# Kernel tuning notes

Measured on AMD Instinct MI355X. Metric: run time of the kernel, lower is better.

## Reference

```python
import jax, jax.numpy as jnp
import numpy as np

DIM = 768
HEADS = 12
HEAD_DIM = DIM // HEADS
SCALE = HEAD_DIM ** -0.5


def setup_inputs() -> dict:
    key = jax.random.key(0)
    ks = jax.random.split(key, 9)
    B, N, M, C = 4, 1024, 1024, DIM
    std = C ** -0.5
    return {
        "q": jax.random.normal(ks[0], (B, N, C), jnp.float32),
        "k": jax.random.normal(ks[1], (B, M, C), jnp.float32),
        "v": jax.random.normal(ks[2], (B, M, C), jnp.float32),
        "mask": jax.random.uniform(ks[3], (B, N, M), jnp.float32),
        "Wq": jax.random.normal(ks[4], (C, C), jnp.float32) * std,
        "Wk": jax.random.normal(ks[5], (C, C), jnp.float32) * std,
        "Wv": jax.random.normal(ks[6], (C, C), jnp.float32) * std,
        "Wp": jax.random.normal(ks[7], (C, C), jnp.float32) * std,
        "bp": jax.random.normal(ks[8], (C,), jnp.float32) * 0.01,
    }


def reference(q, k, v, mask, Wq, Wk, Wv, Wp, bp):
    B, N, C = q.shape
    M = k.shape[1]
    H, D = HEADS, HEAD_DIM
    qh = (q @ Wq).reshape(B, N, H, D)
    kh = (k @ Wk).reshape(B, M, H, D)
    vh = (v @ Wv).reshape(B, M, H, D)
    attn = jnp.einsum('bnhd,bmhd->bhnm', qh, kh) * SCALE
    attn = jax.nn.softmax(attn, axis=-1)
    # post-softmax multiplicative mask, broadcast over heads
    attn = attn * mask[:, None, :, :]
    x = jnp.einsum('bhnm,bmhd->bnhd', attn, vh).reshape(B, N, C)
    return x @ Wp + bp
```

## Files before the change

### kernel.cpp

```cpp
#include <hip/hip_runtime.h>

typedef __bf16 bf16x8 __attribute__((ext_vector_type(8)));
typedef float f32x4 __attribute__((ext_vector_type(4)));

__device__ __forceinline__ unsigned short f2bf(float f) {
  union { float f; unsigned u; } x; x.f = f;
  unsigned r = x.u + 0x7FFFu + ((x.u >> 16) & 1u);
  return (unsigned short)(r >> 16);
}

__device__ __forceinline__ void gload_lds16(const void* g, void* l) {
  __builtin_amdgcn_global_load_lds(
      (const __attribute__((address_space(1))) unsigned int*)g,
      (__attribute__((address_space(3))) unsigned int*)l, 16, 0, 0);
}

__device__ __forceinline__ f32x4 mfma16(bf16x8 a, bf16x8 b, f32x4 c) {
  return __builtin_amdgcn_mfma_f32_16x16x32_bf16(a, b, c, 0, 0, 0);
}

__global__ __launch_bounds__(256) void conv_qkv(const float* __restrict__ q,
                                                const float* __restrict__ k,
                                                const float* __restrict__ v,
                                                unsigned short* __restrict__ dst) {
  const float* src = (blockIdx.y == 0) ? q : (blockIdx.y == 1 ? k : v);
  size_t i = ((size_t)blockIdx.x * 256 + threadIdx.x) * 4;
  float4 f = *(const float4*)(src + i);
  ushort4 u;
  u.x = f2bf(f.x); u.y = f2bf(f.y); u.z = f2bf(f.z); u.w = f2bf(f.w);
  *(ushort4*)(dst + (size_t)blockIdx.y * (4096u * 768u) + i) = u;
}

__global__ __launch_bounds__(256) void conv_w(const float* __restrict__ W0,
                                              const float* __restrict__ W1,
                                              const float* __restrict__ W2,
                                              const float* __restrict__ W3,
                                              unsigned short* __restrict__ Wt) {
  __shared__ float tile[32][33];
  const float* W = (blockIdx.z == 0) ? W0 : (blockIdx.z == 1) ? W1
                   : (blockIdx.z == 2) ? W2 : W3;
  int tx = threadIdx.x, ty = threadIdx.y;
  int n0 = blockIdx.x * 32, k0 = blockIdx.y * 32;
#pragma unroll
  for (int i = 0; i < 4; ++i)
    tile[ty * 4 + i][tx] = W[(size_t)(k0 + ty * 4 + i) * 768 + n0 + tx];
  __syncthreads();
  unsigned short* o = Wt + (size_t)blockIdx.z * 768 * 768;
#pragma unroll
  for (int i = 0; i < 4; ++i)
    o[(size_t)(n0 + ty * 4 + i) * 768 + k0 + tx] = f2bf(tile[tx][ty * 4 + i]);
}

__device__ __forceinline__ void gemm_core(const unsigned short* __restrict__ A,
                                          const unsigned short* __restrict__ B,
                                          unsigned short (*As)[64 * 64],
                                          unsigned short (*Bs)[128 * 64],
                                          int m0, int n0, int wm, int wn,
                                          int t, int g, int c16,
                                          f32x4 (&acc)[2][4]) {
  auto stageA = [&](unsigned short* dst, int k0) {
#pragma unroll
    for (int i = 0; i < 2; ++i) {
      int fc = i * 256 + t, r = fc >> 3, c = (fc & 7) ^ ((r >> 1) & 7);
      gload_lds16(A + (size_t)(m0 + r) * 768 + k0 + c * 8, (char*)dst + fc * 16);
    }
  };
  auto stageB = [&](unsigned short* dst, int k0) {
#pragma unroll
    for (int i = 0; i < 4; ++i) {
      int fc = i * 256 + t, r = fc >> 3, c = (fc & 7) ^ ((r >> 1) & 7);
      gload_lds16(B + (size_t)(n0 + r) * 768 + k0 + c * 8, (char*)dst + fc * 16);
    }
  };
  stageA(As[0], 0);
  stageB(Bs[0], 0);
  asm volatile("s_waitcnt vmcnt(0)" ::: "memory");
  __syncthreads();
  for (int s = 0; s < 12; ++s) {
    const int cur = s & 1;
    if (s < 11) {
      stageA(As[cur ^ 1], (s + 1) * 64);
      stageB(Bs[cur ^ 1], (s + 1) * 64);
    }
#pragma unroll
    for (int kk = 0; kk < 2; ++kk) {
      const int ch = kk * 4 + g;
      bf16x8 a[2], bw[4];
#pragma unroll
      for (int mi = 0; mi < 2; ++mi) {
        int r = wm + mi * 16 + c16;
        a[mi] = *(const bf16x8*)((char*)As[cur] + r * 128 + (((ch ^ (r >> 1)) & 7) << 4));
      }
#pragma unroll
      for (int ni = 0; ni < 4; ++ni) {
        int r = wn + ni * 16 + c16;
        bw[ni] = *(const bf16x8*)((char*)Bs[cur] + r * 128 + (((ch ^ (r >> 1)) & 7) << 4));
      }
#pragma unroll
      for (int mi = 0; mi < 2; ++mi)
#pragma unroll
        for (int ni = 0; ni < 4; ++ni)
          acc[mi][ni] = mfma16(a[mi], bw[ni], acc[mi][ni]);
    }
    __syncthreads();
  }
}

__global__ __launch_bounds__(256) void gemm_qkv(const unsigned short* __restrict__ Abase,
                                                const unsigned short* __restrict__ Wt,
                                                unsigned short* __restrict__ Hq,
                                                unsigned short* __restrict__ Hk,
                                                unsigned short* __restrict__ Hvt) {
  __shared__ unsigned short As[2][64 * 64], Bs[2][128 * 64];
  const int z = blockIdx.z;
  const unsigned short* A = Abase + (size_t)z * 4096 * 768;
  const unsigned short* B = Wt + (size_t)z * 768 * 768;
  const int t = threadIdx.x, l = t & 63, wid = t >> 6;
  const int g = l >> 4, c16 = l & 15;
  const int m0 = blockIdx.y * 64, n0 = blockIdx.x * 128;
  const int wm = (wid >> 1) * 32, wn = (wid & 1) * 64;
  f32x4 acc[2][4] = {};
  gemm_core(A, B, As, Bs, m0, n0, wm, wn, t, g, c16, acc);
  if (z < 2) {
    unsigned short* C = (z == 0) ? Hq : Hk;
#pragma unroll
    for (int mi = 0; mi < 2; ++mi)
#pragma unroll
      for (int ni = 0; ni < 4; ++ni) {
        int col = n0 + wn + ni * 16 + c16;
        int row = m0 + wm + mi * 16 + g * 4;
#pragma unroll
        for (int j = 0; j < 4; ++j)
          C[(size_t)(row + j) * 768 + col] = f2bf(acc[mi][ni][j]);
      }
  } else {
#pragma unroll
    for (int mi = 0; mi < 2; ++mi) {
      int rowbase = m0 + wm + mi * 16;
      int bat = rowbase >> 10;
      int mloc = (rowbase & 1023) + g * 4;
#pragma unroll
      for (int ni = 0; ni < 4; ++ni) {
        int col = n0 + wn + ni * 16 + c16;
        ushort4 u;
        u.x = f2bf(acc[mi][ni][0]); u.y = f2bf(acc[mi][ni][1]);
        u.z = f2bf(acc[mi][ni][2]); u.w = f2bf(acc[mi][ni][3]);
        *(ushort4*)(Hvt + (((size_t)(bat * 768 + col)) << 10) + mloc) = u;
      }
    }
  }
}

__global__ __launch_bounds__(256) void attn(const unsigned short* __restrict__ qh,
                                            const unsigned short* __restrict__ kh,
                                            const unsigned short* __restrict__ vhT,
                                            const float* __restrict__ mask,
                                            unsigned short* __restrict__ xb) {
  __shared__ unsigned short Ks[2][64 * 64], Vts[2][64 * 64], Ps[4 * 16 * 64];
  const int qt = blockIdx.x, h = blockIdx.y, b = blockIdx.z;
  const int t = threadIdx.x, l = t & 63, wid = t >> 6;
  const int g = l >> 4, c16 = l & 15;

  const unsigned short* qp =
      qh + ((size_t)(b * 1024 + qt * 64 + wid * 16 + c16)) * 768 + h * 64 + g * 8;
  bf16x8 aq0 = *(const bf16x8*)qp;
  bf16x8 aq1 = *(const bf16x8*)(qp + 32);

  const int fc0 = t, r0 = fc0 >> 3, c0 = (fc0 & 7) ^ ((r0 >> 1) & 7);
  const int fc1 = 256 + t, r1 = fc1 >> 3, c1 = (fc1 & 7) ^ ((r1 >> 1) & 7);
  const unsigned short* kp0 = kh + (size_t)(b * 1024 + r0) * 768 + h * 64 + c0 * 8;
  const unsigned short* kp1 = kh + (size_t)(b * 1024 + r1) * 768 + h * 64 + c1 * 8;
  const unsigned short* vp0 = vhT + ((size_t)(b * 768 + h * 64 + r0)) * 1024 + c0 * 8;
  const unsigned short* vp1 = vhT + ((size_t)(b * 768 + h * 64 + r1)) * 1024 + c1 * 8;
  gload_lds16(kp0, (char*)Ks[0] + fc0 * 16);
  gload_lds16(kp1, (char*)Ks[0] + fc1 * 16);
  gload_lds16(vp0, (char*)Vts[0] + fc0 * 16);
  gload_lds16(vp1, (char*)Vts[0] + fc1 * 16);
  kp0 += 64 * 768; kp1 += 64 * 768; vp0 += 64; vp1 += 64;

  const float* mrow0 =
      mask + ((size_t)(b * 1024 + qt * 64 + wid * 16 + g * 4)) * 1024 + c16;
  const float* mrow1 = mrow0 + 1024;
  const float* mrow2 = mrow0 + 2048;
  const float* mrow3 = mrow0 + 3072;

  asm volatile("s_waitcnt vmcnt(0)" ::: "memory");
  __syncthreads();

  f32x4 o[4] = {};
  float ls[4] = {0.f, 0.f, 0.f, 0.f};
  const float sc = 0.125f * 1.44269504088896341f;
  char* Pw = (char*)Ps + wid * 2048;

  for (int kv = 0; kv < 16; ++kv) {
    const int cur = kv & 1;
    if (kv < 15) {
      char* kd = (char*)Ks[cur ^ 1];
      char* vd = (char*)Vts[cur ^ 1];
      gload_lds16(kp0, kd + fc0 * 16);
      gload_lds16(kp1, kd + fc1 * 16);
      gload_lds16(vp0, vd + fc0 * 16);
      gload_lds16(vp1, vd + fc1 * 16);
      kp0 += 64 * 768; kp1 += 64 * 768; vp0 += 64; vp1 += 64;
    }
    float mreg[4][4];
#pragma unroll
    for (int ni = 0; ni < 4; ++ni) {
      mreg[ni][0] = mrow0[ni * 16];
      mreg[ni][1] = mrow1[ni * 16];
      mreg[ni][2] = mrow2[ni * 16];
      mreg[ni][3] = mrow3[ni * 16];
    }
    mrow0 += 64; mrow1 += 64; mrow2 += 64; mrow3 += 64;
    f32x4 p[4] = {};
#pragma unroll
    for (int kk = 0; kk < 2; ++kk) {
      const int ch = kk * 4 + g;
      bf16x8 aq = kk ? aq1 : aq0;
#pragma unroll
      for (int ni = 0; ni < 4; ++ni) {
        int r = ni * 16 + c16;
        bf16x8 bk = *(const bf16x8*)((char*)Ks[cur] + r * 128 + (((ch ^ (r >> 1)) & 7) << 4));
        p[ni] = mfma16(aq, bk, p[ni]);
      }
    }
#pragma unroll
    for (int j = 0; j < 4; ++j) {
      float e0 = exp2f(p[0][j] * sc);
      float e1 = exp2f(p[1][j] * sc);
      float e2 = exp2f(p[2][j] * sc);
      float e3 = exp2f(p[3][j] * sc);
      p[0][j] = e0; p[1][j] = e1; p[2][j] = e2; p[3][j] = e3;
      ls[j] += (e0 + e1) + (e2 + e3);
    }
#pragma unroll
    for (int ni = 0; ni < 4; ++ni)
#pragma unroll
      for (int j = 0; j < 4; ++j) {
        float pv = p[ni][j] * mreg[ni][j];
        int row = g * 4 + j, col = ni * 16 + c16;
        *(unsigned short*)(Pw + row * 128 +
                           ((((col >> 3) ^ (row >> 1)) & 7) << 4) + ((col & 7) << 1)) = f2bf(pv);
      }
    asm volatile("s_waitcnt lgkmcnt(0)" ::: "memory");
#pragma unroll
    for (int kk = 0; kk < 2; ++kk) {
      const int ch = kk * 4 + g;
      bf16x8 ap = *(const bf16x8*)(Pw + c16 * 128 + (((ch ^ (c16 >> 1)) & 7) << 4));
#pragma unroll
      for (int ni = 0; ni < 4; ++ni) {
        int r = ni * 16 + c16;
        bf16x8 bv = *(const bf16x8*)((char*)Vts[cur] + r * 128 + (((ch ^ (r >> 1)) & 7) << 4));
        o[ni] = mfma16(ap, bv, o[ni]);
      }
    }
    __syncthreads();
  }
#pragma unroll
  for (int j = 0; j < 4; ++j) {
    float s = ls[j];
    s += __shfl_xor(s, 1);
    s += __shfl_xor(s, 2);
    s += __shfl_xor(s, 4);
    s += __shfl_xor(s, 8);
    ls[j] = 1.0f / s;
  }
#pragma unroll
  for (int ni = 0; ni < 4; ++ni) {
    int col = h * 64 + ni * 16 + c16;
    int row = qt * 64 + wid * 16 + g * 4;
#pragma unroll
    for (int j = 0; j < 4; ++j)
      xb[((size_t)(b * 1024) + row + j) * 768 + col] = f2bf(o[ni][j] * ls[j]);
  }
}

__global__ __launch_bounds__(256) void gemm_proj(const unsigned short* __restrict__ A,
                                                 const unsigned short* __restrict__ B,
                                                 const float* __restrict__ bias,
                                                 float* __restrict__ C) {
  __shared__ unsigned short As[2][64 * 64], Bs[2][128 * 64];
  const int t = threadIdx.x, l = t & 63, wid = t >> 6;
  const int g = l >> 4, c16 = l & 15;
  const int m0 = blockIdx.y * 64, n0 = blockIdx.x * 128;
  const int wm = (wid >> 1) * 32, wn = (wid & 1) * 64;
  f32x4 acc[2][4] = {};
  gemm_core(A, B, As, Bs, m0, n0, wm, wn, t, g, c16, acc);
#pragma unroll
  for (int mi = 0; mi < 2; ++mi)
#pragma unroll
    for (int ni = 0; ni < 4; ++ni) {
      int col = n0 + wn + ni * 16 + c16;
      int row = m0 + wm + mi * 16 + g * 4;
      float bv = bias[col];
#pragma unroll
      for (int j = 0; j < 4; ++j)
        C[(size_t)(row + j) * 768 + col] = acc[mi][ni][j] + bv;
    }
}

extern "C" void kernel_launch(void* const* d_in, const int* in_sizes, int n_in,
                              void* d_out, int out_size, void* d_ws, size_t ws_size,
                              hipStream_t stream) {
  const float* q    = (const float*)d_in[0];
  const float* k    = (const float*)d_in[1];
  const float* v    = (const float*)d_in[2];
  const float* mask = (const float*)d_in[3];
  const float* Wq   = (const float*)d_in[4];
  const float* Wk   = (const float*)d_in[5];
  const float* Wv   = (const float*)d_in[6];
  const float* Wp   = (const float*)d_in[7];
  const float* bp   = (const float*)d_in[8];
  float* out = (float*)d_out;

  const size_t MN = (size_t)4096 * 768;
  const size_t WW = (size_t)768 * 768;
  unsigned short* qkv_bf = (unsigned short*)d_ws;
  unsigned short* wt     = qkv_bf + 3 * MN;
  unsigned short* heads  = wt + 4 * WW;
  unsigned short* xb     = heads + 3 * MN;

  conv_qkv<<<dim3(3072, 3), 256, 0, stream>>>(q, k, v, qkv_bf);
  conv_w<<<dim3(24, 24, 4), dim3(32, 8), 0, stream>>>(Wq, Wk, Wv, Wp, wt);
  gemm_qkv<<<dim3(6, 64, 3), 256, 0, stream>>>(qkv_bf, wt, heads, heads + MN, heads + 2 * MN);
  attn<<<dim3(16, 12, 4), 256, 0, stream>>>(heads, heads + MN, heads + 2 * MN, mask, xb);
  gemm_proj<<<dim3(6, 64), 256, 0, stream>>>(xb, wt + 3 * WW, bp, out);
}
```

Before: 102.8 us.

## Keep softmax probabilities in registers by transposing QK^T MFMA and permuting K rows

Swaps the MFMA operand order so S^T comes out in a register layout that can be packed straight into the A operand of the PV MFMA. K rows are loaded in a permuted order so the keys line up with that layout. This removes the per-iteration LDS write/read round trip through the P buffer. The softmax scale is folded into Q in the projection epilogue, and the mask is now read with vectorised float4 loads. The row-sum reduction is reworked with cross-lane shuffles to match the new layout, which adds index-permutation complexity and a risk of subtle layout errors.

```diff
diff --git a/kernel.cpp b/kernel.cpp
--- a/kernel.cpp
+++ b/kernel.cpp
@@ -17,6 +17,13 @@
 
 __device__ __forceinline__ f32x4 mfma16(bf16x8 a, bf16x8 b, f32x4 c) {
   return __builtin_amdgcn_mfma_f32_16x16x32_bf16(a, b, c, 0, 0, 0);
+}
+
+__device__ __forceinline__ bf16x8 pack8(const f32x4& a, const f32x4& b) {
+  bf16x8 r;
+  r[0] = (__bf16)a[0]; r[1] = (__bf16)a[1]; r[2] = (__bf16)a[2]; r[3] = (__bf16)a[3];
+  r[4] = (__bf16)b[0]; r[5] = (__bf16)b[1]; r[6] = (__bf16)b[2]; r[7] = (__bf16)b[3];
+  return r;
 }
 
 __global__ __launch_bounds__(256) void conv_qkv(const float* __restrict__ q,
@@ -122,6 +129,7 @@
   f32x4 acc[2][4] = {};
   gemm_core(A, B, As, Bs, m0, n0, wm, wn, t, g, c16, acc);
   if (z < 2) {
+    const float f = (z == 0) ? 0.125f * 1.44269504088896341f : 1.0f;
     unsigned short* C = (z == 0) ? Hq : Hk;
 #pragma unroll
     for (int mi = 0; mi < 2; ++mi)
@@ -131,7 +139,7 @@
         int row = m0 + wm + mi * 16 + g * 4;
 #pragma unroll
         for (int j = 0; j < 4; ++j)
-          C[(size_t)(row + j) * 768 + col] = f2bf(acc[mi][ni][j]);
+          C[(size_t)(row + j) * 768 + col] = f2bf(acc[mi][ni][j] * f);
       }
   } else {
 #pragma unroll
@@ -156,7 +164,7 @@
                                             const unsigned short* __restrict__ vhT,
                                             const float* __restrict__ mask,
                                             unsigned short* __restrict__ xb) {
-  __shared__ unsigned short Ks[2][64 * 64], Vts[2][64 * 64], Ps[4 * 16 * 64];
+  __shared__ unsigned short Ks[2][64 * 64], Vts[2][64 * 64];
   const int qt = blockIdx.x, h = blockIdx.y, b = blockIdx.z;
   const int t = threadIdx.x, l = t & 63, wid = t >> 6;
   const int g = l >> 4, c16 = l & 15;
@@ -168,8 +176,10 @@
 
   const int fc0 = t, r0 = fc0 >> 3, c0 = (fc0 & 7) ^ ((r0 >> 1) & 7);
   const int fc1 = 256 + t, r1 = fc1 >> 3, c1 = (fc1 & 7) ^ ((r1 >> 1) & 7);
-  const unsigned short* kp0 = kh + (size_t)(b * 1024 + r0) * 768 + h * 64 + c0 * 8;
-  const unsigned short* kp1 = kh + (size_t)(b * 1024 + r1) * 768 + h * 64 + c1 * 8;
+  const int s0 = 32 * (r0 >> 5) + 8 * ((r0 >> 2) & 3) + 4 * ((r0 >> 4) & 1) + (r0 & 3);
+  const int s1 = 32 * (r1 >> 5) + 8 * ((r1 >> 2) & 3) + 4 * ((r1 >> 4) & 1) + (r1 & 3);
+  const unsigned short* kp0 = kh + (size_t)(b * 1024 + s0) * 768 + h * 64 + c0 * 8;
+  const unsigned short* kp1 = kh + (size_t)(b * 1024 + s1) * 768 + h * 64 + c1 * 8;
   const unsigned short* vp0 = vhT + ((size_t)(b * 768 + h * 64 + r0)) * 1024 + c0 * 8;
   const unsigned short* vp1 = vhT + ((size_t)(b * 768 + h * 64 + r1)) * 1024 + c1 * 8;
   gload_lds16(kp0, (char*)Ks[0] + fc0 * 16);
@@ -178,19 +188,13 @@
   gload_lds16(vp1, (char*)Vts[0] + fc1 * 16);
   kp0 += 64 * 768; kp1 += 64 * 768; vp0 += 64; vp1 += 64;
 
-  const float* mrow0 =
-      mask + ((size_t)(b * 1024 + qt * 64 + wid * 16 + g * 4)) * 1024 + c16;
-  const float* mrow1 = mrow0 + 1024;
-  const float* mrow2 = mrow0 + 2048;
-  const float* mrow3 = mrow0 + 3072;
+  const float* mq = mask + ((size_t)(b * 1024 + qt * 64 + wid * 16 + c16)) * 1024 + 8 * g;
 
   asm volatile("s_waitcnt vmcnt(0)" ::: "memory");
   __syncthreads();
 
   f32x4 o[4] = {};
-  float ls[4] = {0.f, 0.f, 0.f, 0.f};
-  const float sc = 0.125f * 1.44269504088896341f;
-  char* Pw = (char*)Ps + wid * 2048;
+  f32x4 ls = {0.f, 0.f, 0.f, 0.f};
 
   for (int kv = 0; kv < 16; ++kv) {
     const int cur = kv & 1;
@@ -203,15 +207,12 @@
       gload_lds16(vp1, vd + fc1 * 16);
       kp0 += 64 * 768; kp1 += 64 * 768; vp0 += 64; vp1 += 64;
     }
-    float mreg[4][4];
-#pragma unroll
-    for (int ni = 0; ni < 4; ++ni) {
-      mreg[ni][0] = mrow0[ni * 16];
-      mreg[ni][1] = mrow1[ni * 16];
-      mreg[ni][2] = mrow2[ni * 16];
-      mreg[ni][3] = mrow3[ni * 16];
-    }
-    mrow0 += 64; mrow1 += 64; mrow2 += 64; mrow3 += 64;
+    const float* mk = mq + kv * 64;
+    f32x4 mreg[4];
+    mreg[0] = *(const f32x4*)(mk);
+    mreg[1] = *(const f32x4*)(mk + 4);
+    mreg[2] = *(const f32x4*)(mk + 32);
+    mreg[3] = *(const f32x4*)(mk + 36);
     f32x4 p[4] = {};
 #pragma unroll
     for (int kk = 0; kk < 2; ++kk) {
@@ -221,32 +222,27 @@
       for (int ni = 0; ni < 4; ++ni) {
         int r = ni * 16 + c16;
         bf16x8 bk = *(const bf16x8*)((char*)Ks[cur] + r * 128 + (((ch ^ (r >> 1)) & 7) << 4));
-        p[ni] = mfma16(aq, bk, p[ni]);
-      }
-    }
-#pragma unroll
-    for (int j = 0; j < 4; ++j) {
-      float e0 = exp2f(p[0][j] * sc);
-      float e1 = exp2f(p[1][j] * sc);
-      float e2 = exp2f(p[2][j] * sc);
-      float e3 = exp2f(p[3][j] * sc);
-      p[0][j] = e0; p[1][j] = e1; p[2][j] = e2; p[3][j] = e3;
-      ls[j] += (e0 + e1) + (e2 + e3);
-    }
-#pragma unroll
-    for (int ni = 0; ni < 4; ++ni)
-#pragma unroll
-      for (int j = 0; j < 4; ++j) {
-        float pv = p[ni][j] * mreg[ni][j];
-        int row = g * 4 + j, col = ni * 16 + c16;
-        *(unsigned short*)(Pw + row * 128 +
-                           ((((col >> 3) ^ (row >> 1)) & 7) << 4) + ((col & 7) << 1)) = f2bf(pv);
-      }
-    asm volatile("s_waitcnt lgkmcnt(0)" ::: "memory");
+        p[ni] = mfma16(bk, aq, p[ni]);
+      }
+    }
+#pragma unroll
+    for (int ni = 0; ni < 4; ++ni) {
+      float e0 = exp2f(p[ni][0]);
+      float e1 = exp2f(p[ni][1]);
+      float e2 = exp2f(p[ni][2]);
+      float e3 = exp2f(p[ni][3]);
+      ls[ni] += (e0 + e1) + (e2 + e3);
+      p[ni][0] = e0 * mreg[ni][0];
+      p[ni][1] = e1 * mreg[ni][1];
+      p[ni][2] = e2 * mreg[ni][2];
+      p[ni][3] = e3 * mreg[ni][3];
+    }
+    bf16x8 pa0 = pack8(p[0], p[1]);
+    bf16x8 pa1 = pack8(p[2], p[3]);
 #pragma unroll
     for (int kk = 0; kk < 2; ++kk) {
       const int ch = kk * 4 + g;
-      bf16x8 ap = *(const bf16x8*)(Pw + c16 * 128 + (((ch ^ (c16 >> 1)) & 7) << 4));
+      bf16x8 ap = kk ? pa1 : pa0;
 #pragma unroll
       for (int ni = 0; ni < 4; ++ni) {
         int r = ni * 16 + c16;
@@ -256,22 +252,21 @@
     }
     __syncthreads();
   }
-#pragma unroll
-  for (int j = 0; j < 4; ++j) {
-    float s = ls[j];
-    s += __shfl_xor(s, 1);
-    s += __shfl_xor(s, 2);
-    s += __shfl_xor(s, 4);
-    s += __shfl_xor(s, 8);
-    ls[j] = 1.0f / s;
-  }
+  float s = (ls[0] + ls[1]) + (ls[2] + ls[3]);
+  s += __shfl_xor(s, 16);
+  s += __shfl_xor(s, 32);
+  float rinv = 1.0f / s;
+  const int rb = (l & 48) | ((l >> 2) & 12);
+  float rj[4];
+#pragma unroll
+  for (int j = 0; j < 4; ++j) rj[j] = __shfl(rinv, rb + j);
 #pragma unroll
   for (int ni = 0; ni < 4; ++ni) {
     int col = h * 64 + ni * 16 + c16;
     int row = qt * 64 + wid * 16 + g * 4;
 #pragma unroll
     for (int j = 0; j < 4; ++j)
-      xb[((size_t)(b * 1024) + row + j) * 768 + col] = f2bf(o[ni][j] * ls[j]);
+      xb[((size_t)(b * 1024) + row + j) * 768 + col] = f2bf(o[ni][j] * rj[j]);
   }
 }
 
```

Result: slower. 106.7 us (+3.7%).
